# Kernel optimization log

Hardware: AMD Instinct MI355X
Metric: run time of the kernel (lower is better)

## Reference

```python
import jax, jax.numpy as jnp
import numpy as np

N = 50000
E = 800000
IN_CH, HID, OUT_CH = 8, 64, 1
NEG_SLOPE = 0.2


def setup_inputs() -> dict:
    key = jax.random.key(0)
    ks = jax.random.split(key, 16)
    x = jax.random.normal(ks[0], (N, IN_CH), dtype=jnp.float32)
    edge_index = jax.random.randint(ks[1], (2, E), 0, N, dtype=jnp.int64)
    def glorot(k, shape):
        fan = shape[0] + shape[-1]
        return jax.random.uniform(k, shape, jnp.float32, -1.0, 1.0) * jnp.sqrt(6.0 / fan)
    # layer 1: in=8 -> 4 heads x 64, concat=False (mean over heads)
    W1 = glorot(ks[2], (IN_CH, 4 * HID))
    as1 = glorot(ks[3], (4, HID)); ad1 = glorot(ks[4], (4, HID))
    b1 = jnp.zeros((HID,), jnp.float32)
    # layer 2: 64 -> 4 heads x 64
    W2 = glorot(ks[5], (HID, 4 * HID))
    as2 = glorot(ks[6], (4, HID)); ad2 = glorot(ks[7], (4, HID))
    b2 = jnp.zeros((HID,), jnp.float32)
    # layer 3: 64 -> 1 head x 1
    W3 = glorot(ks[8], (HID, OUT_CH))
    as3 = glorot(ks[9], (1, OUT_CH)); ad3 = glorot(ks[10], (1, OUT_CH))
    b3 = jnp.zeros((OUT_CH,), jnp.float32)
    return {"x": x, "edge_index": edge_index,
            "W1": W1, "b1": b1, "as1": as1, "ad1": ad1,
            "W2": W2, "b2": b2, "as2": as2, "ad2": ad2,
            "W3": W3, "b3": b3, "as3": as3, "ad3": ad3}


def gat_conv(x, src, dst, W, b, a_src, a_dst, n_nodes):
    """PyG GATConv, concat=False (mean over heads), add_self_loops already applied."""
    heads, ch = a_src.shape
    h = (x @ W).reshape(n_nodes, heads, ch)            # [N,H,C]
    e_src = jnp.sum(h * a_src[None], axis=-1)          # [N,H]
    e_dst = jnp.sum(h * a_dst[None], axis=-1)          # [N,H]
    logits = jax.nn.leaky_relu(e_src[src] + e_dst[dst], NEG_SLOPE)  # [E,H]
    # softmax over incoming edges of each destination node (self loops ensure non-empty)
    m = jax.ops.segment_max(logits, dst, num_segments=n_nodes)      # [N,H]
    ex = jnp.exp(logits - m[dst])
    denom = jax.ops.segment_sum(ex, dst, num_segments=n_nodes)      # [N,H]
    alpha = ex / (denom[dst] + 1e-16)                  # [E,H]
    out = jax.ops.segment_sum(alpha[:, :, None] * h[src], dst, num_segments=n_nodes)  # [N,H,C]
    return jnp.mean(out, axis=1) + b                   # [N,C]


def reference(x, edge_index, W1, b1, as1, ad1, W2, b2, as2, ad2, W3, b3, as3, ad3):
    n = x.shape[0]
    loops = jnp.arange(n, dtype=edge_index.dtype)
    src = jnp.concatenate([edge_index[0], loops])
    dst = jnp.concatenate([edge_index[1], loops])
    h = jax.nn.elu(gat_conv(x, src, dst, W1, b1, as1, ad1, n))
    # Dropout(p=0.2) is identity in eval mode
    h = jax.nn.elu(gat_conv(h, src, dst, W2, b2, as2, ad2, n))
    out = jax.nn.sigmoid(gat_conv(h, src, dst, W3, b3, as3, ad3, n))
    return out  # [N,1] failure probability per node
```

## Files before the change

### kernel.cpp

```cpp
#include <hip/hip_runtime.h>
#include <hip/hip_bf16.h>
#include <hip/hip_fp16.h>
#include <math.h>

#define N_NODES 50000
#define N_EDGES 800000
#define N_TOT   (N_EDGES + N_NODES)
#define NEG_SLOPE 0.2f

static __device__ __forceinline__ float lrelu(float x){ return x >= 0.f ? x : NEG_SLOPE * x; }

__global__ void k_init(const int* __restrict__ ei, int* __restrict__ flag,
                       int* __restrict__ deg){
  int i = blockIdx.x * blockDim.x + threadIdx.x;
  if (i == 0){
    int o = 0;
    #pragma unroll
    for (int j = 1; j < 16; j += 2) o |= ei[j];
    *flag = (o == 0) ? 1 : 0;
  }
  if (i < N_NODES) deg[i] = 1;
}

__global__ void k_count(const int* __restrict__ ei, const int* __restrict__ flag,
                        int* __restrict__ deg){
  int t = blockIdx.x * blockDim.x + threadIdx.x;
  if (t >= N_EDGES / 2) return;
  int d0, d1;
  if (*flag){
    int4 dv = *(const int4*)&ei[2 * N_EDGES + 4 * t];
    d0 = dv.x; d1 = dv.z;
  } else {
    int2 dv = *(const int2*)&ei[N_EDGES + 2 * t];
    d0 = dv.x; d1 = dv.y;
  }
  atomicAdd(&deg[d0], 1);
  atomicAdd(&deg[d1], 1);
}

__global__ void k_scan1(const int* __restrict__ deg, int* __restrict__ rowptr,
                        int* __restrict__ bsum){
  __shared__ int sd[256];
  int t = threadIdx.x;
  int base = blockIdx.x * 1024 + t * 4;
  int v0 = (base + 0 < N_NODES) ? deg[base + 0] : 0;
  int v1 = (base + 1 < N_NODES) ? deg[base + 1] : 0;
  int v2 = (base + 2 < N_NODES) ? deg[base + 2] : 0;
  int v3 = (base + 3 < N_NODES) ? deg[base + 3] : 0;
  int tsum = v0 + v1 + v2 + v3;
  sd[t] = tsum; __syncthreads();
  for (int off = 1; off < 256; off <<= 1){
    int vv = (t >= off) ? sd[t - off] : 0;
    __syncthreads();
    sd[t] += vv;
    __syncthreads();
  }
  int excl = sd[t] - tsum;
  if (base + 0 < N_NODES) rowptr[base + 0] = excl;
  if (base + 1 < N_NODES) rowptr[base + 1] = excl + v0;
  if (base + 2 < N_NODES) rowptr[base + 2] = excl + v0 + v1;
  if (base + 3 < N_NODES) rowptr[base + 3] = excl + v0 + v1 + v2;
  if (t == 255) bsum[blockIdx.x] = sd[255];
}

#define NB_SCAN 49
__global__ void k_scan2(const int* __restrict__ bsum, int* __restrict__ boff){
  int t = threadIdx.x;
  int v = (t < NB_SCAN) ? bsum[t] : 0;
  int incl = v;
  #pragma unroll
  for (int off = 1; off < 64; off <<= 1){
    int u = __shfl_up(incl, off);
    if (t >= off) incl += u;
  }
  if (t < NB_SCAN) boff[t] = incl - v;
}

__global__ void k_scan3(int* __restrict__ rowptr, const int* __restrict__ boff,
                        int* __restrict__ fill){
  int i = blockIdx.x * blockDim.x + threadIdx.x;
  if (i < N_NODES){
    int v = rowptr[i] + boff[i >> 10];
    rowptr[i] = v;
    fill[i] = v;
  }
  if (i == 0) rowptr[N_NODES] = N_TOT;
}

__global__ void k_scatter(const int* __restrict__ ei, const int* __restrict__ flag,
                          int* __restrict__ fill, int* __restrict__ col){
  int t = blockIdx.x * blockDim.x + threadIdx.x;
  if (t < N_EDGES / 2){
    int s0, s1, d0, d1;
    if (*flag){
      int4 sv = *(const int4*)&ei[4 * t];
      int4 dv = *(const int4*)&ei[2 * N_EDGES + 4 * t];
      s0 = sv.x; s1 = sv.z; d0 = dv.x; d1 = dv.z;
    } else {
      int2 sv = *(const int2*)&ei[2 * t];
      int2 dv = *(const int2*)&ei[N_EDGES + 2 * t];
      s0 = sv.x; s1 = sv.y; d0 = dv.x; d1 = dv.y;
    }
    col[atomicAdd(&fill[d0], 1)] = s0;
    col[atomicAdd(&fill[d1], 1)] = s1;
  } else {
    int n = t - N_EDGES / 2;
    if (n < N_NODES) col[atomicAdd(&fill[n], 1)] = n;
  }
}


__global__ __launch_bounds__(256) void k_transform1(
    const float* __restrict__ xin, const float* __restrict__ W,
    const float* __restrict__ aS, const float* __restrict__ aD,
    __half* __restrict__ h, float* __restrict__ es, float* __restrict__ ed){
  __shared__ float wl[8 * 256];
  int tid = threadIdx.x;
  for (int i = tid; i < 8 * 256; i += 256) wl[i] = W[i];
  int lane = tid & 63, wv = tid >> 6, head = lane >> 4;
  float4 s4 = *(const float4*)&aS[4 * lane];
  float4 d4 = *(const float4*)&aD[4 * lane];
  __syncthreads();
  int base = (blockIdx.x * 4 + wv) * 8;
  for (int m = 0; m < 8; m++){
    int n = base + m;
    if (n >= N_NODES) break;
    float4 xa = *(const float4*)&xin[n * 8];
    float4 xb = *(const float4*)&xin[n * 8 + 4];
    float xs0 = xa.x, xs1 = xa.y, xs2 = xa.z, xs3 = xa.w;
    float xs4 = xb.x, xs5 = xb.y, xs6 = xb.z, xs7 = xb.w;
    float4 acc = make_float4(0.f, 0.f, 0.f, 0.f);
    #define T1STEP(k, xv) { float4 w4 = *(const float4*)&wl[(k)*256 + 4*lane]; \
      acc.x = fmaf(xv, w4.x, acc.x); acc.y = fmaf(xv, w4.y, acc.y); \
      acc.z = fmaf(xv, w4.z, acc.z); acc.w = fmaf(xv, w4.w, acc.w); }
    T1STEP(0, xs0) T1STEP(1, xs1) T1STEP(2, xs2) T1STEP(3, xs3)
    T1STEP(4, xs4) T1STEP(5, xs5) T1STEP(6, xs6) T1STEP(7, xs7)
    #undef T1STEP
    __half2 p0 = __floats2half2_rn(acc.x, acc.y);
    __half2 p1 = __floats2half2_rn(acc.z, acc.w);
    uint2 u; u.x = *(unsigned int*)&p0; u.y = *(unsigned int*)&p1;
    *(uint2*)&h[(size_t)n * 256 + 4 * lane] = u;
    float ps = acc.x*s4.x + acc.y*s4.y + acc.z*s4.z + acc.w*s4.w;
    float pd = acc.x*d4.x + acc.y*d4.y + acc.z*d4.z + acc.w*d4.w;
    #pragma unroll
    for (int off = 1; off < 16; off <<= 1){ ps += __shfl_xor(ps, off); pd += __shfl_xor(pd, off); }
    if ((lane & 15) == 0){ es[n * 4 + head] = ps; ed[n * 4 + head] = pd; }
  }
}

__global__ __launch_bounds__(256) void k_transform2(
    const float* __restrict__ xin, const float* __restrict__ W,
    const float* __restrict__ aS, const float* __restrict__ aD,
    __half* __restrict__ h, float* __restrict__ es, float* __restrict__ ed){
  __shared__ float wl[32 * 256];
  int tid = threadIdx.x;
  int lane = tid & 63, wv = tid >> 6, head = lane >> 4;
  float4 s4 = *(const float4*)&aS[4 * lane];
  float4 d4 = *(const float4*)&aD[4 * lane];
  int base = (blockIdx.x * 4 + wv) * 8;
  float xr[8];
  #pragma unroll
  for (int m = 0; m < 8; m++){
    int n = base + m;
    xr[m] = (n < N_NODES) ? xin[(size_t)n * 64 + lane] : 0.f;
  }
  float4 acc[8];
  #pragma unroll
  for (int m = 0; m < 8; m++) acc[m] = make_float4(0.f, 0.f, 0.f, 0.f);
  for (int hf = 0; hf < 2; hf++){
    if (hf) __syncthreads();
    const float4* Wv = (const float4*)(W + hf * 32 * 256);
    float4* wlv = (float4*)wl;
    #pragma unroll
    for (int i = 0; i < 8; i++) wlv[tid + 256 * i] = Wv[tid + 256 * i];
    __syncthreads();
    #pragma unroll 4
    for (int k = 0; k < 32; k++){
      float4 w4 = *(const float4*)&wl[k * 256 + 4 * lane];
      #pragma unroll
      for (int m = 0; m < 8; m++){
        float xv = __shfl(xr[m], hf * 32 + k);
        acc[m].x = fmaf(xv, w4.x, acc[m].x);
        acc[m].y = fmaf(xv, w4.y, acc[m].y);
        acc[m].z = fmaf(xv, w4.z, acc[m].z);
        acc[m].w = fmaf(xv, w4.w, acc[m].w);
      }
    }
  }
  #pragma unroll
  for (int m = 0; m < 8; m++){
    int n = base + m;
    if (n >= N_NODES) break;
    __half2 p0 = __floats2half2_rn(acc[m].x, acc[m].y);
    __half2 p1 = __floats2half2_rn(acc[m].z, acc[m].w);
    uint2 u; u.x = *(unsigned int*)&p0; u.y = *(unsigned int*)&p1;
    *(uint2*)&h[(size_t)n * 256 + 4 * lane] = u;
    float ps = acc[m].x*s4.x + acc[m].y*s4.y + acc[m].z*s4.z + acc[m].w*s4.w;
    float pd = acc[m].x*d4.x + acc[m].y*d4.y + acc[m].z*d4.z + acc[m].w*d4.w;
    #pragma unroll
    for (int off = 1; off < 16; off <<= 1){ ps += __shfl_xor(ps, off); pd += __shfl_xor(pd, off); }
    if ((lane & 15) == 0){ es[n * 4 + head] = ps; ed[n * 4 + head] = pd; }
  }
}

__global__ __launch_bounds__(256) void k_transform3(
    const float* __restrict__ xin, const float* __restrict__ W3,
    const float* __restrict__ aS, const float* __restrict__ aD,
    float2* __restrict__ pk, float* __restrict__ ed3){
  int gid = blockIdx.x * blockDim.x + threadIdx.x;
  int n = gid >> 6, lane = gid & 63;
  if (n >= N_NODES) return;
  float v = xin[(size_t)n * 64 + lane] * W3[lane];
  #pragma unroll
  for (int off = 1; off < 64; off <<= 1) v += __shfl_xor(v, off);
  if (lane == 0){
    pk[n] = make_float2(v * aS[0], v);
    ed3[n] = v * aD[0];
  }
}

static __device__ __forceinline__ void agg_step(float4& acc, uint2 u, float wt){
  float2 aa = __half22float2(*(__half2*)&u.x);
  float2 bb = __half22float2(*(__half2*)&u.y);
  acc.x = fmaf(wt, aa.x, acc.x); acc.y = fmaf(wt, aa.y, acc.y);
  acc.z = fmaf(wt, bb.x, acc.z); acc.w = fmaf(wt, bb.y, acc.w);
}

__global__ __launch_bounds__(256) void k_agg(
    const __half* __restrict__ h, const float* __restrict__ es, const float* __restrict__ ed,
    const int* __restrict__ rowptr, const int* __restrict__ col,
    const float* __restrict__ bias, float* __restrict__ outf){
  int gid = blockIdx.x * blockDim.x + threadIdx.x;
  int d = gid >> 6, lane = gid & 63;
  if (d >= N_NODES) return;
  int start = rowptr[d], end = rowptr[d + 1];
  int head = lane >> 4;
  float eh = ed[d * 4 + head];
  const __half* hp = h + 4 * lane;
  float4 acc = make_float4(0.f, 0.f, 0.f, 0.f);
  float wsum = 0.f;
  int i = start;
  for (; i + 8 <= end; i += 8){
    int s0 = col[i],     s1 = col[i + 1], s2 = col[i + 2], s3 = col[i + 3];
    int s4 = col[i + 4], s5 = col[i + 5], s6 = col[i + 6], s7 = col[i + 7];
    uint2 u0 = *(const uint2*)(hp + (size_t)s0 * 256);
    uint2 u1 = *(const uint2*)(hp + (size_t)s1 * 256);
    uint2 u2 = *(const uint2*)(hp + (size_t)s2 * 256);
    uint2 u3 = *(const uint2*)(hp + (size_t)s3 * 256);
    uint2 u4 = *(const uint2*)(hp + (size_t)s4 * 256);
    uint2 u5 = *(const uint2*)(hp + (size_t)s5 * 256);
    uint2 u6 = *(const uint2*)(hp + (size_t)s6 * 256);
    uint2 u7 = *(const uint2*)(hp + (size_t)s7 * 256);
    float e0 = es[s0 * 4 + head], e1 = es[s1 * 4 + head];
    float e2 = es[s2 * 4 + head], e3 = es[s3 * 4 + head];
    float e4 = es[s4 * 4 + head], e5 = es[s5 * 4 + head];
    float e6 = es[s6 * 4 + head], e7 = es[s7 * 4 + head];
    float w0 = __expf(lrelu(e0 + eh)), w1 = __expf(lrelu(e1 + eh));
    float w2 = __expf(lrelu(e2 + eh)), w3 = __expf(lrelu(e3 + eh));
    float w4 = __expf(lrelu(e4 + eh)), w5 = __expf(lrelu(e5 + eh));
    float w6 = __expf(lrelu(e6 + eh)), w7 = __expf(lrelu(e7 + eh));
    wsum += ((w0 + w1) + (w2 + w3)) + ((w4 + w5) + (w6 + w7));
    agg_step(acc, u0, w0); agg_step(acc, u1, w1);
    agg_step(acc, u2, w2); agg_step(acc, u3, w3);
    agg_step(acc, u4, w4); agg_step(acc, u5, w5);
    agg_step(acc, u6, w6); agg_step(acc, u7, w7);
  }
  for (; i < end; i++){
    int s0 = col[i];
    uint2 u0 = *(const uint2*)(hp + (size_t)s0 * 256);
    float w0 = __expf(lrelu(es[s0 * 4 + head] + eh));
    wsum += w0;
    agg_step(acc, u0, w0);
  }
  float inv = 1.0f / (wsum + 1e-16f);
  acc.x *= inv; acc.y *= inv; acc.z *= inv; acc.w *= inv;
  #pragma unroll
  for (int off = 16; off < 64; off <<= 1){
    acc.x += __shfl_xor(acc.x, off);
    acc.y += __shfl_xor(acc.y, off);
    acc.z += __shfl_xor(acc.z, off);
    acc.w += __shfl_xor(acc.w, off);
  }
  if (lane < 16){
    float4 b4 = *(const float4*)&bias[4 * lane];
    float ox = 0.25f * acc.x + b4.x;
    float oy = 0.25f * acc.y + b4.y;
    float oz = 0.25f * acc.z + b4.z;
    float ow = 0.25f * acc.w + b4.w;
    ox = ox > 0.f ? ox : expm1f(ox);
    oy = oy > 0.f ? oy : expm1f(oy);
    oz = oz > 0.f ? oz : expm1f(oz);
    ow = ow > 0.f ? ow : expm1f(ow);
    float4 o = make_float4(ox, oy, oz, ow);
    *(float4*)&outf[(size_t)d * 64 + 4 * lane] = o;
  }
}

__global__ __launch_bounds__(256) void k_agg3(
    const float2* __restrict__ pk, const float* __restrict__ ed3,
    const int* __restrict__ rowptr, const int* __restrict__ col,
    const float* __restrict__ b3, float* __restrict__ out){
  int gid = blockIdx.x * blockDim.x + threadIdx.x;
  int wv = gid >> 6, lane = gid & 63;
  int sub = lane >> 4, li = lane & 15;
  int d = wv * 4 + sub;
  if (d < N_NODES){
    int start = rowptr[d], end = rowptr[d + 1];
    float edv = ed3[d];
    float num = 0.f, den = 0.f;
    for (int i = start + li; i < end; i += 16){
      float2 p = pk[col[i]];
      float wgt = __expf(lrelu(p.x + edv));
      den += wgt;
      num = fmaf(wgt, p.y, num);
    }
    #pragma unroll
    for (int off = 1; off < 16; off <<= 1){
      num += __shfl_xor(num, off);
      den += __shfl_xor(den, off);
    }
    if (li == 0){
      float v = num / (den + 1e-16f) + b3[0];
      out[d] = 1.f / (1.f + __expf(-v));
    }
  }
}

extern "C" void kernel_launch(void* const* d_in, const int* in_sizes, int n_in,
                              void* d_out, int out_size, void* d_ws, size_t ws_size,
                              hipStream_t stream) {
  const float* x   = (const float*)d_in[0];
  const int*   ei  = (const int*)  d_in[1];
  const float* W1  = (const float*)d_in[2];
  const float* b1  = (const float*)d_in[3];
  const float* as1 = (const float*)d_in[4];
  const float* ad1 = (const float*)d_in[5];
  const float* W2  = (const float*)d_in[6];
  const float* b2  = (const float*)d_in[7];
  const float* as2 = (const float*)d_in[8];
  const float* ad2 = (const float*)d_in[9];
  const float* W3  = (const float*)d_in[10];
  const float* b3  = (const float*)d_in[11];
  const float* as3 = (const float*)d_in[12];
  const float* ad3 = (const float*)d_in[13];
  float* out = (float*)d_out;

  char* w = (char*)d_ws;
  size_t off = 0;
  auto alloc = [&](size_t bytes) -> char* {
    char* p = w + off;
    off += (bytes + 255) & ~size_t(255);
    return p;
  };
  int*    flag   = (int*)   alloc(64);
  int*    deg    = (int*)   alloc(N_NODES * 4);
  int*    fill   = (int*)   alloc(N_NODES * 4);
  int*    rowptr = (int*)   alloc((N_NODES + 1) * 4);
  int*    bsum   = (int*)   alloc(64 * 4);
  int*    boff   = (int*)   alloc(64 * 4);
  int*    col    = (int*)   alloc((size_t)N_TOT * 4);
  __half* h      = (__half*)alloc((size_t)N_NODES * 256 * 2);
  float*  es     = (float*) alloc((size_t)N_NODES * 4 * 4);
  float*  ed     = (float*) alloc((size_t)N_NODES * 4 * 4);
  float*  feat1  = (float*) alloc((size_t)N_NODES * 64 * 4);
  float*  feat2  = (float*) alloc((size_t)N_NODES * 64 * 4);
  float2* pk     = (float2*)alloc((size_t)N_NODES * 8);
  float*  ed3    = (float*) alloc(N_NODES * 4);
  (void)ws_size; (void)in_sizes; (void)n_in; (void)out_size;

  k_init   <<<(N_NODES + 255) / 256, 256, 0, stream>>>(ei, flag, deg);
  k_count  <<<(N_EDGES / 2 + 255) / 256, 256, 0, stream>>>(ei, flag, deg);
  k_scan1  <<<NB_SCAN, 256, 0, stream>>>(deg, rowptr, bsum);
  k_scan2  <<<1, 64, 0, stream>>>(bsum, boff);
  k_scan3  <<<(N_NODES + 255) / 256, 256, 0, stream>>>(rowptr, boff, fill);
  k_scatter<<<(N_EDGES / 2 + N_NODES + 255) / 256, 256, 0, stream>>>(ei, flag, fill, col);

  const int grid_t12 = (N_NODES + 31) / 32;
  const int grid_wpn = (N_NODES * 64 + 255) / 256;
  const int grid_w4n = ((N_NODES + 3) / 4 * 64 + 255) / 256;

  k_transform1<<<grid_t12, 256, 0, stream>>>(x, W1, as1, ad1, h, es, ed);
  k_agg       <<<grid_wpn, 256, 0, stream>>>(h, es, ed, rowptr, col, b1, feat1);
  k_transform2<<<grid_t12, 256, 0, stream>>>(feat1, W2, as2, ad2, h, es, ed);
  k_agg       <<<grid_wpn, 256, 0, stream>>>(h, es, ed, rowptr, col, b2, feat2);
  k_transform3<<<grid_wpn, 256, 0, stream>>>(feat2, W3, as3, ad3, pk, ed3);
  k_agg3      <<<grid_w4n, 256, 0, stream>>>(pk, ed3, rowptr, col, b3, out);
}
```

Baseline: 408.7 us.

## Fold block-offset scan into scan3, widen edge loads, shrink agg unroll

Removes the single-block k_scan2 launch by having every k_scan3 block recompute the 49-entry block-offset scan in shared memory. k_count and k_scatter now handle four edges per thread with wider int4 loads, which halves their thread counts. The k_agg neighbor loop is unrolled by 4 instead of 8, trading memory-level parallelism for lower register pressure and a shorter remainder loop. Each k_scan3 block redundantly reads bsum and runs a wavefront scan, and fewer outstanding gathers per lane in k_agg could expose more latency.

```diff
diff --git a/kernel.cpp b/kernel.cpp
--- a/kernel.cpp
+++ b/kernel.cpp
@@ -25,17 +25,20 @@
 __global__ void k_count(const int* __restrict__ ei, const int* __restrict__ flag,
                         int* __restrict__ deg){
   int t = blockIdx.x * blockDim.x + threadIdx.x;
-  if (t >= N_EDGES / 2) return;
-  int d0, d1;
+  if (t >= N_EDGES / 4) return;
+  int d0, d1, d2, d3;
   if (*flag){
-    int4 dv = *(const int4*)&ei[2 * N_EDGES + 4 * t];
-    d0 = dv.x; d1 = dv.z;
+    int4 a = *(const int4*)&ei[2 * N_EDGES + 8 * t];
+    int4 b = *(const int4*)&ei[2 * N_EDGES + 8 * t + 4];
+    d0 = a.x; d1 = a.z; d2 = b.x; d3 = b.z;
   } else {
-    int2 dv = *(const int2*)&ei[N_EDGES + 2 * t];
-    d0 = dv.x; d1 = dv.y;
+    int4 a = *(const int4*)&ei[N_EDGES + 4 * t];
+    d0 = a.x; d1 = a.y; d2 = a.z; d3 = a.w;
   }
   atomicAdd(&deg[d0], 1);
   atomicAdd(&deg[d1], 1);
+  atomicAdd(&deg[d2], 1);
+  atomicAdd(&deg[d3], 1);
 }
 
 __global__ void k_scan1(const int* __restrict__ deg, int* __restrict__ rowptr,
@@ -64,23 +67,24 @@
 }
 
 #define NB_SCAN 49
-__global__ void k_scan2(const int* __restrict__ bsum, int* __restrict__ boff){
+__global__ void k_scan3(int* __restrict__ rowptr, const int* __restrict__ bsum,
+                        int* __restrict__ fill){
+  __shared__ int sboff[64];
   int t = threadIdx.x;
-  int v = (t < NB_SCAN) ? bsum[t] : 0;
-  int incl = v;
-  #pragma unroll
-  for (int off = 1; off < 64; off <<= 1){
-    int u = __shfl_up(incl, off);
-    if (t >= off) incl += u;
-  }
-  if (t < NB_SCAN) boff[t] = incl - v;
-}
-
-__global__ void k_scan3(int* __restrict__ rowptr, const int* __restrict__ boff,
-                        int* __restrict__ fill){
-  int i = blockIdx.x * blockDim.x + threadIdx.x;
+  if (t < 64){
+    int v = (t < NB_SCAN) ? bsum[t] : 0;
+    int incl = v;
+    #pragma unroll
+    for (int off = 1; off < 64; off <<= 1){
+      int u = __shfl_up(incl, off);
+      if (t >= off) incl += u;
+    }
+    sboff[t] = incl - v;
+  }
+  __syncthreads();
+  int i = blockIdx.x * blockDim.x + t;
   if (i < N_NODES){
-    int v = rowptr[i] + boff[i >> 10];
+    int v = rowptr[i] + sboff[i >> 10];
     rowptr[i] = v;
     fill[i] = v;
   }
@@ -90,21 +94,27 @@
 __global__ void k_scatter(const int* __restrict__ ei, const int* __restrict__ flag,
                           int* __restrict__ fill, int* __restrict__ col){
   int t = blockIdx.x * blockDim.x + threadIdx.x;
-  if (t < N_EDGES / 2){
-    int s0, s1, d0, d1;
+  if (t < N_EDGES / 4){
+    int s0, s1, s2, s3, d0, d1, d2, d3;
     if (*flag){
-      int4 sv = *(const int4*)&ei[4 * t];
-      int4 dv = *(const int4*)&ei[2 * N_EDGES + 4 * t];
-      s0 = sv.x; s1 = sv.z; d0 = dv.x; d1 = dv.z;
+      int4 sa = *(const int4*)&ei[8 * t];
+      int4 sb = *(const int4*)&ei[8 * t + 4];
+      int4 da = *(const int4*)&ei[2 * N_EDGES + 8 * t];
+      int4 db = *(const int4*)&ei[2 * N_EDGES + 8 * t + 4];
+      s0 = sa.x; s1 = sa.z; s2 = sb.x; s3 = sb.z;
+      d0 = da.x; d1 = da.z; d2 = db.x; d3 = db.z;
     } else {
-      int2 sv = *(const int2*)&ei[2 * t];
-      int2 dv = *(const int2*)&ei[N_EDGES + 2 * t];
-      s0 = sv.x; s1 = sv.y; d0 = dv.x; d1 = dv.y;
+      int4 sa = *(const int4*)&ei[4 * t];
+      int4 da = *(const int4*)&ei[N_EDGES + 4 * t];
+      s0 = sa.x; s1 = sa.y; s2 = sa.z; s3 = sa.w;
+      d0 = da.x; d1 = da.y; d2 = da.z; d3 = da.w;
     }
     col[atomicAdd(&fill[d0], 1)] = s0;
     col[atomicAdd(&fill[d1], 1)] = s1;
+    col[atomicAdd(&fill[d2], 1)] = s2;
+    col[atomicAdd(&fill[d3], 1)] = s3;
   } else {
-    int n = t - N_EDGES / 2;
+    int n = t - N_EDGES / 4;
     if (n < N_NODES) col[atomicAdd(&fill[n], 1)] = n;
   }
 }
@@ -240,30 +250,21 @@
   float4 acc = make_float4(0.f, 0.f, 0.f, 0.f);
   float wsum = 0.f;
   int i = start;
-  for (; i + 8 <= end; i += 8){
-    int s0 = col[i],     s1 = col[i + 1], s2 = col[i + 2], s3 = col[i + 3];
-    int s4 = col[i + 4], s5 = col[i + 5], s6 = col[i + 6], s7 = col[i + 7];
+  for (; i + 4 <= end; i += 4){
+    int s0 = col[i], s1 = col[i + 1], s2 = col[i + 2], s3 = col[i + 3];
     uint2 u0 = *(const uint2*)(hp + (size_t)s0 * 256);
     uint2 u1 = *(const uint2*)(hp + (size_t)s1 * 256);
     uint2 u2 = *(const uint2*)(hp + (size_t)s2 * 256);
     uint2 u3 = *(const uint2*)(hp + (size_t)s3 * 256);
-    uint2 u4 = *(const uint2*)(hp + (size_t)s4 * 256);
-    uint2 u5 = *(const uint2*)(hp + (size_t)s5 * 256);
-    uint2 u6 = *(const uint2*)(hp + (size_t)s6 * 256);
-    uint2 u7 = *(const uint2*)(hp + (size_t)s7 * 256);
     float e0 = es[s0 * 4 + head], e1 = es[s1 * 4 + head];
     float e2 = es[s2 * 4 + head], e3 = es[s3 * 4 + head];
-    float e4 = es[s4 * 4 + head], e5 = es[s5 * 4 + head];
-    float e6 = es[s6 * 4 + head], e7 = es[s7 * 4 + head];
-    float w0 = __expf(lrelu(e0 + eh)), w1 = __expf(lrelu(e1 + eh));
-    float w2 = __expf(lrelu(e2 + eh)), w3 = __expf(lrelu(e3 + eh));
-    float w4 = __expf(lrelu(e4 + eh)), w5 = __expf(lrelu(e5 + eh));
-    float w6 = __expf(lrelu(e6 + eh)), w7 = __expf(lrelu(e7 + eh));
-    wsum += ((w0 + w1) + (w2 + w3)) + ((w4 + w5) + (w6 + w7));
+    float w0 = __expf(lrelu(e0 + eh));
+    float w1 = __expf(lrelu(e1 + eh));
+    float w2 = __expf(lrelu(e2 + eh));
+    float w3 = __expf(lrelu(e3 + eh));
+    wsum += (w0 + w1) + (w2 + w3);
     agg_step(acc, u0, w0); agg_step(acc, u1, w1);
     agg_step(acc, u2, w2); agg_step(acc, u3, w3);
-    agg_step(acc, u4, w4); agg_step(acc, u5, w5);
-    agg_step(acc, u6, w6); agg_step(acc, u7, w7);
   }
   for (; i < end; i++){
     int s0 = col[i];
@@ -357,7 +358,6 @@
   int*    fill   = (int*)   alloc(N_NODES * 4);
   int*    rowptr = (int*)   alloc((N_NODES + 1) * 4);
   int*    bsum   = (int*)   alloc(64 * 4);
-  int*    boff   = (int*)   alloc(64 * 4);
   int*    col    = (int*)   alloc((size_t)N_TOT * 4);
   __half* h      = (__half*)alloc((size_t)N_NODES * 256 * 2);
   float*  es     = (float*) alloc((size_t)N_NODES * 4 * 4);
@@ -369,11 +369,10 @@
   (void)ws_size; (void)in_sizes; (void)n_in; (void)out_size;
 
   k_init   <<<(N_NODES + 255) / 256, 256, 0, stream>>>(ei, flag, deg);
-  k_count  <<<(N_EDGES / 2 + 255) / 256, 256, 0, stream>>>(ei, flag, deg);
+  k_count  <<<(N_EDGES / 4 + 255) / 256, 256, 0, stream>>>(ei, flag, deg);
   k_scan1  <<<NB_SCAN, 256, 0, stream>>>(deg, rowptr, bsum);
-  k_scan2  <<<1, 64, 0, stream>>>(bsum, boff);
-  k_scan3  <<<(N_NODES + 255) / 256, 256, 0, stream>>>(rowptr, boff, fill);
-  k_scatter<<<(N_EDGES / 2 + N_NODES + 255) / 256, 256, 0, stream>>>(ei, flag, fill, col);
+  k_scan3  <<<(N_NODES + 255) / 256, 256, 0, stream>>>(rowptr, bsum, fill);
+  k_scatter<<<(N_EDGES / 4 + N_NODES + 255) / 256, 256, 0, stream>>>(ei, flag, fill, col);
 
   const int grid_t12 = (N_NODES + 31) / 32;
   const int grid_wpn = (N_NODES * 64 + 255) / 256;
```

New measurement: 394.0 us. 1.04x faster.
